# Performance work log

Hardware: AMD Instinct MI355X
Metric: run time of the kernel (lower is better)

Reference implementation:

```python
import jax, jax.numpy as jnp
import numpy as np

B, S, V, D, H, L = 4, 1024, 32000, 256, 8, 4
DH = D // H  # per-head dim (D_H == F_H since F=D)
EPS = 1e-5


def _layernorm(x, g, b):
    m = jnp.mean(x, axis=-1, keepdims=True)
    v = jnp.mean((x - m) ** 2, axis=-1, keepdims=True)
    return (x - m) * jax.lax.rsqrt(v + EPS) * g + b


def _forward(X, emb, WQ, WK, WV, O, ln_g, ln_b, w1, b1, w2, b2, w3, b3, logitW):
    x = emb[X]  # [B,S,D]
    scale = 1.0 / np.sqrt(DH).astype(np.float32)
    nlayers = WQ.shape[0]
    for i in range(nlayers):
        xn = _layernorm(x, ln_g[i], ln_b[i])
        xh = xn.reshape(B, S, H, DH)  # [B,S,H,DH]
        # repeated 'dd'/'ff' indices extract the DIAGONAL of the per-head weights
        scores = jnp.einsum('bqhd,hdd,bkhd,hdd->bhqk', xh, WQ[i], xh, WK[i]) * scale
        attn = jax.nn.softmax(scores, axis=-1)  # [B,H,S,S]
        y = jnp.einsum('bhqk,bkhf,hff->bqhf', attn, xh, WV[i]).reshape(B, S, D)
        y = jnp.einsum('bqf,ff->bqf', y, O[i])  # diagonal output scaling
        y = jax.nn.gelu(y @ w1[i] + b1[i], approximate=False)
        y = jax.nn.gelu(y @ w2[i] + b2[i], approximate=False)
        y = y @ w3[i] + b3[i]
        x = x + y
    return jnp.einsum('bqd,dt->bqt', x, logitW)  # [B,S,V]


def setup_inputs() -> dict:
    key = jax.random.key(0)
    ks = jax.random.split(key, 16)

    def xavier(k, shape, fan_in, fan_out):
        std = np.sqrt(2.0 / (fan_in + fan_out)).astype(np.float32)
        return jax.random.normal(k, shape, jnp.float32) * std

    inp = {
        'X': jax.random.randint(ks[0], (B, S), 0, V, dtype=jnp.int64),
        'emb': jax.random.normal(ks[1], (V, D), jnp.float32),
        'WQ': xavier(ks[2], (L, H, DH, DH), DH, DH),
        'WK': xavier(ks[3], (L, H, DH, DH), DH, DH),
        'WV': xavier(ks[4], (L, H, DH, DH), DH, DH),
        'O': xavier(ks[5], (L, D, D), D, D),
        'ln_g': jnp.ones((L, D), jnp.float32),
        'ln_b': jnp.zeros((L, D), jnp.float32),
        'w1': xavier(ks[6], (L, D, D), D, D),
        'b1': jnp.zeros((L, D), jnp.float32),
        'w2': xavier(ks[7], (L, D, D), D, D),
        'b2': jnp.zeros((L, D), jnp.float32),
        'w3': xavier(ks[8], (L, D, D), D, D),
        'b3': jnp.zeros((L, D), jnp.float32),
        'logitW': xavier(ks[9], (D, V), D, V),
    }
    return inp


def reference(X, emb, WQ, WK, WV, O, ln_g, ln_b, w1, b1, w2, b2, w3, b3, logitW):
    return _forward(X, emb, WQ, WK, WV, O, ln_g, ln_b, w1, b1, w2, b2, w3, b3, logitW)
```

## Files before the change

kernel.cpp:

```cpp
#include <hip/hip_runtime.h>
#include <hip/hip_bf16.h>
#include <cstdint>
#include <cstddef>

#define B_ 4
#define S_ 1024
#define V_ 32000
#define D_ 256
#define H_ 8
#define DH_ 32
#define L_ 4
#define MROWS (B_*S_)

typedef __attribute__((ext_vector_type(8))) short bf16x8;
typedef __attribute__((ext_vector_type(4))) float f32x4;

__device__ __forceinline__ unsigned short f2bf(float f) {
  union { float f; unsigned u; } c; c.f = f;
  unsigned u = c.u;
  u += 0x7fff + ((u >> 16) & 1);
  return (unsigned short)(u >> 16);
}
__device__ __forceinline__ float bf2f(unsigned short u) {
  union { unsigned u; float f; } c; c.u = ((unsigned)u) << 16; return c.f;
}

__device__ __forceinline__ void gload16(const unsigned short* g, unsigned short* l) {
  __builtin_amdgcn_global_load_lds(
      (const __attribute__((address_space(1))) void*)g,
      (__attribute__((address_space(3))) void*)l, 16, 0, 0);
}

template<int BM, int BK, int NW>
__device__ __forceinline__ void stage_tile_swz(const unsigned short* __restrict__ g, int ldg,
                                               unsigned short* lds, int wave, int lane) {
  constexpr int CH  = BM * BK * 2 / 1024;
  constexpr int BKB = BK * 2;
#pragma unroll
  for (int t = 0; t < CH / NW; ++t) {
    int c = wave + t * NW;
    int byte  = c * 1024 + lane * 16;
    int row   = byte / BKB;
    int inner = (byte % BKB) ^ ((row & 7) << 4);
    gload16(g + (size_t)row * ldg + (inner >> 1), lds + c * 512);
  }
}

template<int BKB>
__device__ __forceinline__ bf16x8 lds_frag(const unsigned short* base, int row, int kbytes) {
  int b = (row * BKB + kbytes) ^ ((row & 7) << 4);
  return *(const bf16x8*)((const char*)base + b);
}

__global__ __launch_bounds__(512) void k_embln(
    const int* __restrict__ X, const float* __restrict__ emb,
    const float* __restrict__ lng, const float* __restrict__ lnb,
    float* __restrict__ x, unsigned short* __restrict__ xbf,
    unsigned short* __restrict__ xnT) {
  __shared__ __align__(16) float xf[16][264];
  __shared__ float mrow[16], rrow[16];
  int r0 = blockIdx.x * 16;
  int tid = threadIdx.x;
  int w = tid >> 6, lane = tid & 63;
#pragma unroll
  for (int rr = 0; rr < 2; rr++) {
    int row = w * 2 + rr; int grow = r0 + row;
    int tok = X[grow];
    f32x4 v = *(const f32x4*)(emb + (size_t)tok * D_ + lane * 4);
    *(f32x4*)(x + (size_t)grow * D_ + lane * 4) = v;
    *(f32x4*)&xf[row][lane * 4] = v;
    float s = v[0] + v[1] + v[2] + v[3];
    float ss = v[0]*v[0] + v[1]*v[1] + v[2]*v[2] + v[3]*v[3];
#pragma unroll
    for (int off = 1; off < 64; off <<= 1) {
      s  += __shfl_xor(s, off, 64);
      ss += __shfl_xor(ss, off, 64);
    }
    float mean = s * (1.f / D_);
    float var = ss * (1.f / D_) - mean * mean;
    float rinv = rsqrtf(var + 1e-5f);
    float4 g4 = *(const float4*)(lng + lane * 4);
    float4 b4 = *(const float4*)(lnb + lane * 4);
    ushort4 o;
    o.x = f2bf((v[0] - mean) * rinv * g4.x + b4.x);
    o.y = f2bf((v[1] - mean) * rinv * g4.y + b4.y);
    o.z = f2bf((v[2] - mean) * rinv * g4.z + b4.z);
    o.w = f2bf((v[3] - mean) * rinv * g4.w + b4.w);
    *(ushort4*)(xbf + (size_t)grow * D_ + lane * 4) = o;
    if (lane == 0) { mrow[row] = mean; rrow[row] = rinv; }
  }
  __syncthreads();
  int d = tid & 255, half = tid >> 8;
  float gd = lng[d], bd = lnb[d];
  int bb = r0 >> 10, s0 = r0 & 1023;
  bf16x8 o8;
#pragma unroll
  for (int k = 0; k < 8; k++) {
    int srow = half * 8 + k;
    o8[k] = (short)f2bf((xf[srow][d] - mrow[srow]) * rrow[srow] * gd + bd);
  }
  *(bf16x8*)(xnT + ((size_t)(bb * 256 + d)) * S_ + s0 + half * 8) = o8;
}

template<int LAST>
__global__ __launch_bounds__(512) void k_layer(
    const unsigned short* __restrict__ xbf,
    const unsigned short* __restrict__ xnT,
    const float* __restrict__ WQ, const float* __restrict__ WK,
    const float* __restrict__ WV, const float* __restrict__ Om,
    const unsigned short* __restrict__ Wl,
    const float* __restrict__ b1, const float* __restrict__ b2, const float* __restrict__ b3,
    float* __restrict__ x,
    const float* __restrict__ lngN, const float* __restrict__ lnbN,
    unsigned short* __restrict__ xbfN, unsigned short* __restrict__ xnTN,
    unsigned short* __restrict__ actB,
    int layer) {
  __shared__ __align__(16) unsigned short P_lds[8][16][72];
  __shared__ __align__(16) unsigned short Aa[16 * 256];
  __shared__ __align__(16) unsigned short Ab[16 * 256];
  __shared__ __align__(16) unsigned short Ab2[16 * 256];
  __shared__ __align__(16) unsigned short Bp[2][256 * 64];
  __shared__ __align__(16) float xf[16][264];
  __shared__ float mrow[16], rrow[16];

  int b = blockIdx.x >> 6;
  int q0 = (blockIdx.x & 63) << 4;
  int r0 = blockIdx.x * 16;
  int tid = threadIdx.x;
  int w = tid >> 6, lane = tid & 63;
  int lr = lane & 15, lg = lane >> 4;
  int h = w;

  stage_tile_swz<256, 64, 8>(Wl, 256, Bp[0], w, lane);

  const float scale = 0.17677669529663687f;
  bf16x8 aq;
  {
    bf16x8 xq = *(const bf16x8*)(xbf + ((size_t)(b * S_ + q0 + lr)) * D_ + h * DH_ + lg * 8);
#pragma unroll
    for (int j = 0; j < 8; j++) {
      int dj = lg * 8 + j;
      float wq = WQ[((size_t)(layer * H_ + h)) * 1024 + dj * 33];
      float wk = WK[((size_t)(layer * H_ + h)) * 1024 + dj * 33];
      aq[j] = (short)f2bf(bf2f((unsigned short)xq[j]) * wq * wk * scale);
    }
  }
  float dvo[2];
#pragma unroll
  for (int fs = 0; fs < 2; fs++) {
    int fh = fs * 16 + lr;
    int fc = h * DH_ + fh;
    dvo[fs] = WV[((size_t)(layer * H_ + h)) * 1024 + fh * 33] *
              Om[(size_t)layer * 65536 + (size_t)fc * 257];
  }

  f32x4 accPV[2];
  accPV[0] = (f32x4){0.f, 0.f, 0.f, 0.f};
  accPV[1] = (f32x4){0.f, 0.f, 0.f, 0.f};
  float rsum[4] = {0.f, 0.f, 0.f, 0.f};

  const unsigned short* xk_base = xbf + ((size_t)b * S_) * D_ + h * DH_ + lg * 8;
  const unsigned short* vT_base = xnT + ((size_t)(b * D_ + h * DH_)) * S_;

  bf16x8 qkb[4];
#pragma unroll
  for (int c = 0; c < 4; c++)
    qkb[c] = *(const bf16x8*)(xk_base + (size_t)(c * 16 + lr) * D_);

  for (int kt = 0; kt < 16; kt++) {
    int k0 = kt * 64;
    bf16x8 pvb[2][2];
#pragma unroll
    for (int fs = 0; fs < 2; fs++)
#pragma unroll
      for (int kc = 0; kc < 2; kc++)
        pvb[fs][kc] = *(const bf16x8*)(vT_base + (size_t)(fs * 16 + lr) * S_ +
                                       k0 + kc * 32 + lg * 8);
    f32x4 s[4];
#pragma unroll
    for (int c = 0; c < 4; c++)
      s[c] = __builtin_amdgcn_mfma_f32_16x16x32_bf16(aq, qkb[c],
                (f32x4){0.f, 0.f, 0.f, 0.f}, 0, 0, 0);
    int ktn = kt < 15 ? kt + 1 : 15;
#pragma unroll
    for (int c = 0; c < 4; c++)
      qkb[c] = *(const bf16x8*)(xk_base + (size_t)(ktn * 64 + c * 16 + lr) * D_);
#pragma unroll
    for (int c = 0; c < 4; c++)
#pragma unroll
      for (int r = 0; r < 4; r++) {
        float p = __expf(s[c][r]);
        rsum[r] += p;
        P_lds[w][lg * 4 + r][c * 16 + lr] = f2bf(p);
      }
#pragma unroll
    for (int kc = 0; kc < 2; kc++) {
      bf16x8 pa = *(const bf16x8*)(&P_lds[w][lr][kc * 32 + lg * 8]);
#pragma unroll
      for (int fs = 0; fs < 2; fs++)
        accPV[fs] = __builtin_amdgcn_mfma_f32_16x16x32_bf16(pa, pvb[fs][kc],
                       accPV[fs], 0, 0, 0);
    }
  }

  float inv[4];
#pragma unroll
  for (int r = 0; r < 4; r++) {
    float v = rsum[r];
    v += __shfl_xor(v, 1, 64);
    v += __shfl_xor(v, 2, 64);
    v += __shfl_xor(v, 4, 64);
    v += __shfl_xor(v, 8, 64);
    inv[r] = 1.f / v;
  }
#pragma unroll
  for (int fs = 0; fs < 2; fs++)
#pragma unroll
    for (int r = 0; r < 4; r++) {
      float val = accPV[fs][r] * inv[r] * dvo[fs];
      int row = lg * 4 + r, col = h * DH_ + fs * 16 + lr;
      int byte = (row * 512 + col * 2) ^ ((row & 7) << 4);
      *(unsigned short*)((char*)Aa + byte) = f2bf(val);
    }
  __syncthreads();

  int lr16 = lr;
  f32x4 acc[2];
  acc[0] = (f32x4){0.f, 0.f, 0.f, 0.f};
  acc[1] = (f32x4){0.f, 0.f, 0.f, 0.f};
  const unsigned short* Asrc = Aa;

  for (int p = 0; p < 12; ++p) {
    if (p < 11) {
      int pn = p + 1;
      stage_tile_swz<256, 64, 8>(Wl + (size_t)(pn >> 2) * 65536 + (pn & 3) * 64,
                                 256, Bp[pn & 1], w, lane);
    }
    int kk0 = (p & 3) * 64;
#pragma unroll
    for (int kk = 0; kk < 64; kk += 32) {
      bf16x8 a = lds_frag<512>(Asrc, lr16, (kk0 + kk) * 2 + lg * 16);
#pragma unroll
      for (int j = 0; j < 2; j++) {
        bf16x8 bfg = lds_frag<128>(Bp[p & 1], w * 32 + j * 16 + lr16, kk * 2 + lg * 16);
        acc[j] = __builtin_amdgcn_mfma_f32_16x16x32_bf16(a, bfg, acc[j], 0, 0, 0);
      }
    }
    if (p == 3 || p == 7) {
      const float* bias = (p == 3) ? b1 : b2;
      unsigned short* dst = (p == 3) ? Ab : Ab2;
#pragma unroll
      for (int j = 0; j < 2; j++) {
        int col = w * 32 + j * 16 + lr16;
        float bv = bias[col];
#pragma unroll
        for (int r = 0; r < 4; r++) {
          float v = acc[j][r] + bv;
          v = 0.5f * v * (1.f + erff(v * 0.70710678118654752f));
          int row = lg * 4 + r;
          int byte = (row * 512 + col * 2) ^ ((row & 7) << 4);
          *(unsigned short*)((char*)dst + byte) = f2bf(v);
        }
      }
      acc[0] = (f32x4){0.f, 0.f, 0.f, 0.f};
      acc[1] = (f32x4){0.f, 0.f, 0.f, 0.f};
      Asrc = (p == 3) ? Ab : Ab2;
    }
    __syncthreads();
  }

#pragma unroll
  for (int j = 0; j < 2; j++) {
    int col = w * 32 + j * 16 + lr16;
    float bv = b3[col];
#pragma unroll
    for (int r = 0; r < 4; r++) {
      int row = lg * 4 + r; int grow = r0 + row;
      float v = acc[j][r] + bv + x[(size_t)grow * D_ + col];
      if constexpr (LAST) {
        actB[(size_t)grow * D_ + col] = f2bf(v);
      } else {
        x[(size_t)grow * D_ + col] = v;
        xf[row][col] = v;
      }
    }
  }

  if constexpr (!LAST) {
    __syncthreads();
#pragma unroll
    for (int rr = 0; rr < 2; rr++) {
      int row = w * 2 + rr; int grow = r0 + row;
      f32x4 v = *(const f32x4*)&xf[row][lane * 4];
      float s = v[0] + v[1] + v[2] + v[3];
      float ss = v[0]*v[0] + v[1]*v[1] + v[2]*v[2] + v[3]*v[3];
#pragma unroll
      for (int off = 1; off < 64; off <<= 1) {
        s  += __shfl_xor(s, off, 64);
        ss += __shfl_xor(ss, off, 64);
      }
      float mean = s * (1.f / D_);
      float var = ss * (1.f / D_) - mean * mean;
      float rinv = rsqrtf(var + 1e-5f);
      float4 g4 = *(const float4*)(lngN + lane * 4);
      float4 b4 = *(const float4*)(lnbN + lane * 4);
      ushort4 o;
      o.x = f2bf((v[0] - mean) * rinv * g4.x + b4.x);
      o.y = f2bf((v[1] - mean) * rinv * g4.y + b4.y);
      o.z = f2bf((v[2] - mean) * rinv * g4.z + b4.z);
      o.w = f2bf((v[3] - mean) * rinv * g4.w + b4.w);
      *(ushort4*)(xbfN + (size_t)grow * D_ + lane * 4) = o;
      if (lane == 0) { mrow[row] = mean; rrow[row] = rinv; }
    }
    __syncthreads();
    int d = tid & 255, half = tid >> 8;
    float gd = lngN[d], bd = lnbN[d];
    int bb = r0 >> 10, s0 = r0 & 1023;
    bf16x8 o8;
#pragma unroll
    for (int k = 0; k < 8; k++) {
      int srow = half * 8 + k;
      o8[k] = (short)f2bf((xf[srow][d] - mrow[srow]) * rrow[srow] * gd + bd);
    }
    *(bf16x8*)(xnTN + ((size_t)(bb * 256 + d)) * S_ + s0 + half * 8) = o8;
  }
}

__global__ __launch_bounds__(512) void k_logits(
    const unsigned short* __restrict__ A,
    const float* __restrict__ logitW,
    float* __restrict__ C) {
  __shared__ __align__(16) unsigned short Bs[128 * 256];
  __shared__ __align__(16) unsigned short As[2][64 * 256];

  int tid = threadIdx.x, lane = tid & 63, w = tid >> 6;
  int wm = w >> 2, wn = w & 3;
  int lr = lane & 15, lg = lane >> 4;
  int bn0 = blockIdx.x * 128;

  stage_tile_swz<64, 256, 8>(A, 256, As[0], w, lane);

  {
    int c = tid & 127;
    int kp = tid >> 7;
    for (int it = 0; it < 32; ++it) {
      int k = it * 8 + kp * 2;
      float f0 = logitW[(size_t)k * V_ + bn0 + c];
      float f1 = logitW[(size_t)(k + 1) * V_ + bn0 + c];
      unsigned pack = (unsigned)f2bf(f0) | ((unsigned)f2bf(f1) << 16);
      int byte = (c * 512 + k * 2) ^ ((c & 7) << 4);
      *(unsigned*)((char*)Bs + byte) = pack;
    }
  }
  __syncthreads();

  bf16x8 breg[2][8];
#pragma unroll
  for (int j = 0; j < 2; j++)
#pragma unroll
    for (int ks = 0; ks < 8; ks++)
      breg[j][ks] = lds_frag<512>(Bs, wn * 32 + j * 16 + lr, ks * 64 + lg * 16);

  for (int t = 0; t < 64; ++t) {
    int cur = t & 1;
    if (t < 63)
      stage_tile_swz<64, 256, 8>(A + (size_t)(t + 1) * 64 * 256, 256, As[cur ^ 1], w, lane);

    f32x4 acc[2][2];
#pragma unroll
    for (int i = 0; i < 2; i++)
#pragma unroll
      for (int j = 0; j < 2; j++) acc[i][j] = (f32x4){0.f, 0.f, 0.f, 0.f};

#pragma unroll
    for (int ks = 0; ks < 8; ks++) {
      bf16x8 af[2];
#pragma unroll
      for (int i = 0; i < 2; i++)
        af[i] = lds_frag<512>(As[cur], wm * 32 + i * 16 + lr, ks * 64 + lg * 16);
#pragma unroll
      for (int i = 0; i < 2; i++)
#pragma unroll
        for (int j = 0; j < 2; j++)
          acc[i][j] = __builtin_amdgcn_mfma_f32_16x16x32_bf16(breg[j][ks], af[i], acc[i][j], 0, 0, 0);
    }

    int r0 = t * 64;
#pragma unroll
    for (int i = 0; i < 2; i++)
#pragma unroll
      for (int j = 0; j < 2; j++) {
        int row = r0 + wm * 32 + i * 16 + lr;
        int colb = bn0 + wn * 32 + j * 16 + lg * 4;
        __builtin_nontemporal_store(acc[i][j], (f32x4*)(C + (size_t)row * V_ + colb));
      }
    __syncthreads();
  }
}

__device__ __forceinline__ void tconv_tile(const float* __restrict__ in,
                                           unsigned short* __restrict__ out,
                                           int R, int C, int r0, int c0, int t) {
  __shared__ float tile[64][65];
#pragma unroll
  for (int i = 0; i < 16; i++) {
    int idx = i * 256 + t;
    int lr = idx >> 6, lc = idx & 63;
    tile[lr][lc] = in[(size_t)(r0 + lr) * C + c0 + lc];
  }
  __syncthreads();
#pragma unroll
  for (int i = 0; i < 16; i++) {
    int idx = i * 256 + t;
    int lr = idx >> 6, lc = idx & 63;
    out[(size_t)(c0 + lr) * R + r0 + lc] = f2bf(tile[lc][lr]);
  }
}

__global__ __launch_bounds__(256) void k_tconv_mlp(const float* __restrict__ w1,
                                                   const float* __restrict__ w2,
                                                   const float* __restrict__ w3,
                                                   unsigned short* __restrict__ out) {
  int z = blockIdx.z; int l = z / 3, mm = z % 3;
  const float* in = (mm == 0 ? w1 : mm == 1 ? w2 : w3) + (size_t)l * 65536;
  tconv_tile(in, out + (size_t)z * 65536, 256, 256, blockIdx.y * 64, blockIdx.x * 64, threadIdx.x);
}

extern "C" void kernel_launch(void* const* d_in, const int* in_sizes, int n_in,
                              void* d_out, int out_size, void* d_ws, size_t ws_size,
                              hipStream_t stream) {
  const int*   X      = (const int*)d_in[0];
  const float* emb    = (const float*)d_in[1];
  const float* WQ     = (const float*)d_in[2];
  const float* WK     = (const float*)d_in[3];
  const float* WV     = (const float*)d_in[4];
  const float* Om     = (const float*)d_in[5];
  const float* lng    = (const float*)d_in[6];
  const float* lnb    = (const float*)d_in[7];
  const float* w1     = (const float*)d_in[8];
  const float* b1     = (const float*)d_in[9];
  const float* w2     = (const float*)d_in[10];
  const float* b2     = (const float*)d_in[11];
  const float* w3     = (const float*)d_in[12];
  const float* b3     = (const float*)d_in[13];
  const float* logitW = (const float*)d_in[14];
  float* out = (float*)d_out;
  char* ws = (char*)d_ws;

  constexpr size_t MB = 1024u * 1024;
  float* x  = (float*)(ws);
  unsigned short* xbf0 = (unsigned short*)(ws + 4 * MB);
  unsigned short* xbf1 = (unsigned short*)(ws + 6 * MB);
  unsigned short* xnT0 = (unsigned short*)(ws + 8 * MB);
  unsigned short* xnT1 = (unsigned short*)(ws + 10 * MB);
  unsigned short* actB = (unsigned short*)(ws + 12 * MB);
  unsigned short* mlpW = (unsigned short*)(ws + 14 * MB);

  k_tconv_mlp<<<dim3(4, 4, 12), 256, 0, stream>>>(w1, w2, w3, mlpW);

  k_embln<<<256, 512, 0, stream>>>(X, emb, lng, lnb, x, xbf0, xnT0);

  for (int l = 0; l < L_; l++) {
    const unsigned short* xbfI = (l & 1) ? xbf1 : xbf0;
    const unsigned short* xnTI = (l & 1) ? xnT1 : xnT0;
    unsigned short* xbfO = (l & 1) ? xbf0 : xbf1;
    unsigned short* xnTO = (l & 1) ? xnT0 : xnT1;
    if (l < L_ - 1) {
      k_layer<0><<<256, 512, 0, stream>>>(
          xbfI, xnTI, WQ, WK, WV, Om, mlpW + (size_t)(l * 3) * 65536,
          b1 + (size_t)l * D_, b2 + (size_t)l * D_, b3 + (size_t)l * D_, x,
          lng + (size_t)(l + 1) * D_, lnb + (size_t)(l + 1) * D_,
          xbfO, xnTO, nullptr, l);
    } else {
      k_layer<1><<<256, 512, 0, stream>>>(
          xbfI, xnTI, WQ, WK, WV, Om, mlpW + (size_t)(l * 3) * 65536,
          b1 + (size_t)l * D_, b2 + (size_t)l * D_, b3 + (size_t)l * D_, x,
          nullptr, nullptr, nullptr, nullptr, actB, l);
    }
  }

  k_logits<<<250, 512, 0, stream>>>(actB, logitW, out);
}
```

Before: 335.3 us.

## Read MLP weight fragments directly from global memory instead of LDS staging

The three chained MLP matmuls in the fused layer kernel now load their bf16 weight fragments straight from global memory (expected to hit L2) into registers, instead of double-buffering weight tiles through shared memory. This drops the 64 KB Bp LDS buffer, which can allow more blocks per CU, and removes the per-stage syncthreads, leaving only two barriers between matmuls. In exchange every wave issues global loads with no explicit prefetch, so MFMA may stall on memory latency. It also depends on the stage_tile_swz layout matching plain row-major indexing.

New measurement: 349.6 us. 1.04x slower.

```diff
diff --git a/kernel.cpp b/kernel.cpp
--- a/kernel.cpp
+++ b/kernel.cpp
@@ -119,7 +119,6 @@
   __shared__ __align__(16) unsigned short Aa[16 * 256];
   __shared__ __align__(16) unsigned short Ab[16 * 256];
   __shared__ __align__(16) unsigned short Ab2[16 * 256];
-  __shared__ __align__(16) unsigned short Bp[2][256 * 64];
   __shared__ __align__(16) float xf[16][264];
   __shared__ float mrow[16], rrow[16];
 
@@ -131,8 +130,6 @@
   int lr = lane & 15, lg = lane >> 4;
   int h = w;
 
-  stage_tile_swz<256, 64, 8>(Wl, 256, Bp[0], w, lane);
-
   const float scale = 0.17677669529663687f;
   bf16x8 aq;
   {
@@ -224,54 +221,50 @@
     }
   __syncthreads();
 
-  int lr16 = lr;
   f32x4 acc[2];
-  acc[0] = (f32x4){0.f, 0.f, 0.f, 0.f};
-  acc[1] = (f32x4){0.f, 0.f, 0.f, 0.f};
-  const unsigned short* Asrc = Aa;
-
-  for (int p = 0; p < 12; ++p) {
-    if (p < 11) {
-      int pn = p + 1;
-      stage_tile_swz<256, 64, 8>(Wl + (size_t)(pn >> 2) * 65536 + (pn & 3) * 64,
-                                 256, Bp[pn & 1], w, lane);
-    }
-    int kk0 = (p & 3) * 64;
-#pragma unroll
-    for (int kk = 0; kk < 64; kk += 32) {
-      bf16x8 a = lds_frag<512>(Asrc, lr16, (kk0 + kk) * 2 + lg * 16);
-#pragma unroll
-      for (int j = 0; j < 2; j++) {
-        bf16x8 bfg = lds_frag<128>(Bp[p & 1], w * 32 + j * 16 + lr16, kk * 2 + lg * 16);
-        acc[j] = __builtin_amdgcn_mfma_f32_16x16x32_bf16(a, bfg, acc[j], 0, 0, 0);
-      }
-    }
-    if (p == 3 || p == 7) {
-      const float* bias = (p == 3) ? b1 : b2;
-      unsigned short* dst = (p == 3) ? Ab : Ab2;
-#pragma unroll
-      for (int j = 0; j < 2; j++) {
-        int col = w * 32 + j * 16 + lr16;
-        float bv = bias[col];
-#pragma unroll
-        for (int r = 0; r < 4; r++) {
-          float v = acc[j][r] + bv;
-          v = 0.5f * v * (1.f + erff(v * 0.70710678118654752f));
-          int row = lg * 4 + r;
-          int byte = (row * 512 + col * 2) ^ ((row & 7) << 4);
-          *(unsigned short*)((char*)dst + byte) = f2bf(v);
-        }
-      }
-      acc[0] = (f32x4){0.f, 0.f, 0.f, 0.f};
-      acc[1] = (f32x4){0.f, 0.f, 0.f, 0.f};
-      Asrc = (p == 3) ? Ab : Ab2;
-    }
-    __syncthreads();
-  }
+  const unsigned short* Wp;
+
+#define MLP_MM(Asrc, WPTR)                                                        \
+  acc[0] = (f32x4){0.f, 0.f, 0.f, 0.f};                                           \
+  acc[1] = (f32x4){0.f, 0.f, 0.f, 0.f};                                           \
+  Wp = (WPTR);                                                                    \
+  _Pragma("unroll")                                                               \
+  for (int k0 = 0; k0 < 256; k0 += 32) {                                          \
+    bf16x8 a = lds_frag<512>(Asrc, lr, k0 * 2 + lg * 16);                         \
+    _Pragma("unroll")                                                             \
+    for (int j = 0; j < 2; j++) {                                                 \
+      bf16x8 bfg = *(const bf16x8*)(Wp + (size_t)(w * 32 + j * 16 + lr) * 256 +   \
+                                    k0 + lg * 8);                                 \
+      acc[j] = __builtin_amdgcn_mfma_f32_16x16x32_bf16(a, bfg, acc[j], 0, 0, 0);  \
+    }                                                                             \
+  }
+
+#define EPI_GELU(bias, dst)                                                       \
+  _Pragma("unroll")                                                               \
+  for (int j = 0; j < 2; j++) {                                                   \
+    int col = w * 32 + j * 16 + lr;                                               \
+    float bv = (bias)[col];                                                       \
+    _Pragma("unroll")                                                             \
+    for (int r = 0; r < 4; r++) {                                                 \
+      float v = acc[j][r] + bv;                                                   \
+      v = 0.5f * v * (1.f + erff(v * 0.70710678118654752f));                      \
+      int row = lg * 4 + r;                                                       \
+      int byte = (row * 512 + col * 2) ^ ((row & 7) << 4);                        \
+      *(unsigned short*)((char*)(dst) + byte) = f2bf(v);                          \
+    }                                                                             \
+  }
+
+  MLP_MM(Aa, Wl)
+  EPI_GELU(b1, Ab)
+  __syncthreads();
+  MLP_MM(Ab, Wl + 65536)
+  EPI_GELU(b2, Ab2)
+  __syncthreads();
+  MLP_MM(Ab2, Wl + 2 * 65536)
 
 #pragma unroll
   for (int j = 0; j < 2; j++) {
-    int col = w * 32 + j * 16 + lr16;
+    int col = w * 32 + j * 16 + lr;
     float bv = b3[col];
 #pragma unroll
     for (int r = 0; r < 4; r++) {
@@ -324,6 +317,8 @@
     }
     *(bf16x8*)(xnTN + ((size_t)(bb * 256 + d)) * S_ + s0 + half * 8) = o8;
   }
+#undef MLP_MM
+#undef EPI_GELU
 }
 
 __global__ __launch_bounds__(512) void k_logits(
```
